# Optimization experiments

Hardware: AMD Instinct MI355X
Metric: run time of the kernel (lower is better)

The kernel has to match this reference:

```python
import jax, jax.numpy as jnp
import numpy as np


def _gnn_layer(feat, W, b, src, dst, n_nodes):
    # edge-wise: gather src feats -> Linear -> scatter-sum at dst
    m = feat @ W + b                                   # [N, out]
    agg = jax.ops.segment_sum(m[src], dst, num_segments=n_nodes)  # [N, out]
    # concat aggregated messages with self-transformed features -> 2*out
    return jnp.concatenate([agg, m], axis=-1)


def setup_inputs() -> dict:
    key = jax.random.key(0)
    ks = jax.random.split(key, 6)
    N, E, D_IN, D_OUT = 50000, 800000, 128, 128
    features = jax.random.normal(ks[0], (N, D_IN), dtype=jnp.float32)
    src = jax.random.randint(ks[1], (E,), 0, N, dtype=jnp.int32)
    dst = jax.random.randint(ks[2], (E,), 0, N, dtype=jnp.int32)
    W1 = jax.random.normal(ks[3], (D_IN, D_OUT), dtype=jnp.float32) / np.sqrt(D_IN)
    b1 = jnp.zeros((D_OUT,), dtype=jnp.float32)
    W2 = jax.random.normal(ks[4], (2 * D_OUT, D_OUT), dtype=jnp.float32) / np.sqrt(2 * D_OUT)
    b2 = jnp.zeros((D_OUT,), dtype=jnp.float32)
    return {"features": features, "src": src, "dst": dst,
            "W1": W1, "b1": b1, "W2": W2, "b2": b2}


def reference(features, src, dst, W1, b1, W2, b2):
    n_nodes = features.shape[0]
    feat = _gnn_layer(features, W1, b1, src, dst, n_nodes)  # [N, 2*out]
    feat = _gnn_layer(feat, W2, b2, src, dst, n_nodes)      # [N, 2*out]
    return feat
```

## Files before the change

### kernel.cpp

```cpp
#include <hip/hip_runtime.h>


#define D 128
#define CBLK 256
#define DCAP 8192

typedef __attribute__((ext_vector_type(8))) short short8;
typedef __attribute__((ext_vector_type(4))) float float4v;
typedef unsigned short ushort_t;
typedef unsigned int uint_t;

static __device__ __forceinline__ ushort_t f2bf(float f) {
    uint_t u = __builtin_bit_cast(uint_t, f);
    u += 0x7FFFu + ((u >> 16) & 1u);
    return (ushort_t)(u >> 16);
}
static __device__ __forceinline__ float bfhi(uint_t u) {
    return __builtin_bit_cast(float, u & 0xFFFF0000u);
}
static __device__ __forceinline__ float bflo(uint_t u) {
    return __builtin_bit_cast(float, u << 16);
}

__global__ __launch_bounds__(256) void pack_w(const float* __restrict__ W1,
                                              const float* __restrict__ W2,
                                              ushort_t* __restrict__ W1p,
                                              ushort_t* __restrict__ W2p) {
    const int n1 = 4 * 8 * 64;
    const int n2 = 8 * 8 * 64;
    int t = blockIdx.x * 256 + threadIdx.x;
    if (t >= n1 + n2) return;
    const float* W; ushort_t* Wp; int tt;
    if (t < n1) { W = W1; Wp = W1p; tt = t; }
    else        { W = W2; Wp = W2p; tt = t - n1; }
    int lane = tt & 63, cg = (tt >> 6) & 7, kb = tt >> 9;
    int krow = kb * 32 + (lane >> 4) * 8;
    int col  = cg * 16 + (lane & 15);
    #pragma unroll
    for (int j = 0; j < 8; ++j)
        Wp[(size_t)tt * 8 + j] = f2bf(W[(size_t)(krow + j) * D + col]);
}

__global__ __launch_bounds__(256) void binA(const int* __restrict__ dst,
                                            int* __restrict__ mat, int E, int NB) {
    __shared__ int h[256];
    const int c = blockIdx.x;
    for (int i = threadIdx.x; i < NB; i += 256) h[i] = 0;
    __syncthreads();
    const int chunk = (E + CBLK - 1) / CBLK;
    int e0 = c * chunk, e1 = e0 + chunk; if (e1 > E) e1 = E;
    for (int e = e0 + threadIdx.x; e < e1; e += 256)
        atomicAdd(&h[dst[e] >> 8], 1);
    __syncthreads();
    for (int i = threadIdx.x; i < NB; i += 256)
        mat[i * CBLK + c] = h[i];
}

__global__ __launch_bounds__(256) void binB1(const int* __restrict__ mat,
                                             int* __restrict__ bb,
                                             int* __restrict__ offs,
                                             int E, int N, int NB) {
    __shared__ int s[256];
    int tid = threadIdx.x;
    int v = 0;
    if (tid < NB) {
        const int* row = &mat[tid * CBLK];
        for (int c = 0; c < CBLK; ++c) v += row[c];
    }
    s[tid] = v; __syncthreads();
    for (int o = 1; o < 256; o <<= 1) {
        int t = (tid >= o) ? s[tid - o] : 0;
        __syncthreads();
        s[tid] += t;
        __syncthreads();
    }
    if (tid < NB) bb[tid] = s[tid] - v;
    if (tid == 0) { bb[NB] = E; offs[N] = E; }
}

__global__ __launch_bounds__(256) void binB2(int* __restrict__ mat,
                                             const int* __restrict__ bb, int NB) {
    __shared__ int s[256];
    int b = blockIdx.x;
    int tid = threadIdx.x;
    int v = mat[b * CBLK + tid];
    s[tid] = v; __syncthreads();
    for (int o = 1; o < 256; o <<= 1) {
        int t = (tid >= o) ? s[tid - o] : 0;
        __syncthreads();
        s[tid] += t;
        __syncthreads();
    }
    mat[b * CBLK + tid] = bb[b] + s[tid] - v;
}

__global__ __launch_bounds__(256) void binC(const int* __restrict__ src,
                                            const int* __restrict__ dst,
                                            const int* __restrict__ mat,
                                            int2* __restrict__ tmp, int E, int NB) {
    __shared__ int base[256];
    __shared__ int lcnt[256];
    const int c = blockIdx.x;
    for (int i = threadIdx.x; i < NB; i += 256) {
        base[i] = mat[i * CBLK + c];
        lcnt[i] = 0;
    }
    __syncthreads();
    const int chunk = (E + CBLK - 1) / CBLK;
    int e0 = c * chunk, e1 = e0 + chunk; if (e1 > E) e1 = E;
    for (int e = e0 + threadIdx.x; e < e1; e += 256) {
        int d = dst[e];
        int b = d >> 8;
        int p = base[b] + atomicAdd(&lcnt[b], 1);
        int2 pr; pr.x = d; pr.y = src[e];
        tmp[p] = pr;
    }
}

__global__ __launch_bounds__(256) void binD(const int2* __restrict__ tmp,
                                            const int* __restrict__ bb,
                                            int* __restrict__ offs,
                                            int* __restrict__ bsrc, int N, int NB) {
    __shared__ int hist[256];
    __shared__ int foff[256];
    __shared__ int cntf[256];
    __shared__ int outS[DCAP];
    const int b = blockIdx.x;
    const int tid = threadIdx.x;
    const int beg = bb[b], end = bb[b + 1];
    const int cnt = end - beg;
    const int n0 = b << 8;

    hist[tid] = 0;
    __syncthreads();
    for (int i = tid; i < cnt; i += 256)
        atomicAdd(&hist[tmp[beg + i].x & 255], 1);
    __syncthreads();
    int v = hist[tid];
    int s = v;
    __syncthreads();
    hist[tid] = s; __syncthreads();
    for (int o = 1; o < 256; o <<= 1) {
        int t = (tid >= o) ? hist[tid - o] : 0;
        __syncthreads();
        hist[tid] += t;
        __syncthreads();
    }
    foff[tid] = hist[tid] - v;
    cntf[tid] = 0;
    __syncthreads();

    int node = n0 + tid;
    if (node < N) offs[node] = beg + foff[tid];

    if (cnt <= DCAP) {
        for (int i = tid; i < cnt; i += 256) {
            int2 p = tmp[beg + i];
            int f = p.x & 255;
            int pos = foff[f] + atomicAdd(&cntf[f], 1);
            outS[pos] = p.y;
        }
        __syncthreads();
        for (int i = tid; i < cnt; i += 256)
            bsrc[beg + i] = outS[i];
    } else {
        for (int i = tid; i < cnt; i += 256) {
            int2 p = tmp[beg + i];
            int f = p.x & 255;
            int pos = foff[f] + atomicAdd(&cntf[f], 1);
            bsrc[beg + pos] = p.y;
        }
    }
}

__global__ __launch_bounds__(256) void gemm1_mfma(
    const float* __restrict__ X, const ushort_t* __restrict__ Wp,
    const float* __restrict__ bias, ushort_t* __restrict__ Ybf, int N)
{
    const int wave = threadIdx.x >> 6;
    const int lane = threadIdx.x & 63;
    const int quad = lane >> 4;
    const int l16  = lane & 15;
    const int r0   = blockIdx.x * 128 + wave * 32;

    float4v acc[2][8];
    #pragma unroll
    for (int cg = 0; cg < 8; ++cg) {
        float bv = bias[cg * 16 + l16];
        float4v b4 = {bv, bv, bv, bv};
        acc[0][cg] = b4; acc[1][cg] = b4;
    }

    const short8* wp8 = (const short8*)Wp;

    #pragma unroll
    for (int kb = 0; kb < 4; ++kb) {
        const int k0 = kb * 32 + quad * 8;
        short8 a[2];
        #pragma unroll
        for (int rb = 0; rb < 2; ++rb) {
            int row = r0 + rb * 16 + l16;
            if (row >= N) row = N - 1;
            const float* p = &X[(size_t)row * D + k0];
            float4 x0 = *(const float4*)p;
            float4 x1 = *(const float4*)(p + 4);
            short8 s;
            s[0] = (short)f2bf(x0.x); s[1] = (short)f2bf(x0.y);
            s[2] = (short)f2bf(x0.z); s[3] = (short)f2bf(x0.w);
            s[4] = (short)f2bf(x1.x); s[5] = (short)f2bf(x1.y);
            s[6] = (short)f2bf(x1.z); s[7] = (short)f2bf(x1.w);
            a[rb] = s;
        }
        #pragma unroll
        for (int cg = 0; cg < 8; ++cg) {
            short8 b = wp8[(kb * 8 + cg) * 64 + lane];
            acc[0][cg] = __builtin_amdgcn_mfma_f32_16x16x32_bf16(a[0], b, acc[0][cg], 0, 0, 0);
            acc[1][cg] = __builtin_amdgcn_mfma_f32_16x16x32_bf16(a[1], b, acc[1][cg], 0, 0, 0);
        }
    }

    #pragma unroll
    for (int rb = 0; rb < 2; ++rb) {
        int rowb = r0 + rb * 16 + quad * 4;
        #pragma unroll
        for (int cg = 0; cg < 8; ++cg) {
            int col = cg * 16 + l16;
            #pragma unroll
            for (int i = 0; i < 4; ++i) {
                int row = rowb + i;
                if (row < N) Ybf[(size_t)row * D + col] = f2bf(acc[rb][cg][i]);
            }
        }
    }
}

__global__ __launch_bounds__(256) void gemm2_mfma(
    const ushort_t* __restrict__ A0, const ushort_t* __restrict__ A1,
    const ushort_t* __restrict__ Wp, const float* __restrict__ bias,
    float* __restrict__ Yf, ushort_t* __restrict__ Ybf, int N)
{
    const int wave = threadIdx.x >> 6;
    const int lane = threadIdx.x & 63;
    const int quad = lane >> 4;
    const int l16  = lane & 15;
    const int r0   = blockIdx.x * 128 + wave * 32;

    float4v acc[2][8];
    #pragma unroll
    for (int cg = 0; cg < 8; ++cg) {
        float bv = bias[cg * 16 + l16];
        float4v b4 = {bv, bv, bv, bv};
        acc[0][cg] = b4; acc[1][cg] = b4;
    }

    const short8* wp8 = (const short8*)Wp;

    #pragma unroll
    for (int kb = 0; kb < 8; ++kb) {
        const ushort_t* __restrict__ A = (kb < 4) ? A0 : A1;
        const int k0 = (kb & 3) * 32 + quad * 8;
        short8 a[2];
        #pragma unroll
        for (int rb = 0; rb < 2; ++rb) {
            int row = r0 + rb * 16 + l16;
            if (row >= N) row = N - 1;
            a[rb] = *(const short8*)&A[(size_t)row * D + k0];
        }
        #pragma unroll
        for (int cg = 0; cg < 8; ++cg) {
            short8 b = wp8[(kb * 8 + cg) * 64 + lane];
            acc[0][cg] = __builtin_amdgcn_mfma_f32_16x16x32_bf16(a[0], b, acc[0][cg], 0, 0, 0);
            acc[1][cg] = __builtin_amdgcn_mfma_f32_16x16x32_bf16(a[1], b, acc[1][cg], 0, 0, 0);
        }
    }

    #pragma unroll
    for (int rb = 0; rb < 2; ++rb) {
        int rowb = r0 + rb * 16 + quad * 4;
        #pragma unroll
        for (int cg = 0; cg < 8; ++cg) {
            int col = cg * 16 + l16;
            #pragma unroll
            for (int i = 0; i < 4; ++i) {
                int row = rowb + i;
                if (row < N) {
                    float v = acc[rb][cg][i];
                    Yf[(size_t)row * 256 + col] = v;
                    Ybf[(size_t)row * D + col] = f2bf(v);
                }
            }
        }
    }
}

__global__ __launch_bounds__(256) void gather_bf(
    const ushort_t* __restrict__ msg,
    const int* __restrict__ offs, const int* __restrict__ bsrc,
    ushort_t* __restrict__ aggB,
    float* __restrict__ aggF,
    int N)
{
    int node = (blockIdx.x * 256 + threadIdx.x) >> 6;
    int lane = threadIdx.x & 63;
    if (node >= N) return;
    const int quad = lane >> 4;
    const int c16  = lane & 15;
    int beg = offs[node], end = offs[node + 1];

    float ax[4] = {0.f, 0.f, 0.f, 0.f};
    float ay[4] = {0.f, 0.f, 0.f, 0.f};
    const uint4* mp = (const uint4*)msg;

    for (int base = beg; base < end; base += 64) {
        int cnt = end - base; if (cnt > 64) cnt = 64;
        int sidx = bsrc[base + (lane < cnt ? lane : cnt - 1)];
        for (int j0 = 0; j0 < cnt; j0 += 16) {
            #pragma unroll
            for (int t = 0; t < 4; ++t) {
                int e  = j0 + t * 4 + quad;
                int ec = (e < cnt) ? e : cnt - 1;
                int s  = __shfl(sidx, ec, 64);
                uint4 u = mp[(size_t)s * 16 + c16];
                if (e < cnt) {
                    ax[0] += bflo(u.x); ay[0] += bfhi(u.x);
                    ax[1] += bflo(u.y); ay[1] += bfhi(u.y);
                    ax[2] += bflo(u.z); ay[2] += bfhi(u.z);
                    ax[3] += bflo(u.w); ay[3] += bfhi(u.w);
                }
            }
        }
    }

    #pragma unroll
    for (int k = 0; k < 4; ++k) {
        ax[k] += __shfl_xor(ax[k], 16, 64);
        ax[k] += __shfl_xor(ax[k], 32, 64);
        ay[k] += __shfl_xor(ay[k], 16, 64);
        ay[k] += __shfl_xor(ay[k], 32, 64);
    }

    if (quad == 0) {
        if (aggB) {
            uint4 o;
            o.x = (uint_t)f2bf(ax[0]) | ((uint_t)f2bf(ay[0]) << 16);
            o.y = (uint_t)f2bf(ax[1]) | ((uint_t)f2bf(ay[1]) << 16);
            o.z = (uint_t)f2bf(ax[2]) | ((uint_t)f2bf(ay[2]) << 16);
            o.w = (uint_t)f2bf(ax[3]) | ((uint_t)f2bf(ay[3]) << 16);
            ((uint4*)aggB)[(size_t)node * 16 + c16] = o;
        } else {
            float4 w0 = {ax[0], ay[0], ax[1], ay[1]};
            float4 w1 = {ax[2], ay[2], ax[3], ay[3]};
            float* p = &aggF[(size_t)node * 256 + c16 * 8];
            *(float4*)p = w0;
            *(float4*)(p + 4) = w1;
        }
    }
}

extern "C" void kernel_launch(void* const* d_in, const int* in_sizes, int n_in,
                              void* d_out, int out_size, void* d_ws, size_t ws_size,
                              hipStream_t stream) {
    const float* features = (const float*)d_in[0];
    const int*   src      = (const int*)d_in[1];
    const int*   dst      = (const int*)d_in[2];
    const float* W1       = (const float*)d_in[3];
    const float* b1       = (const float*)d_in[4];
    const float* W2       = (const float*)d_in[5];
    const float* b2       = (const float*)d_in[6];
    float* out = (float*)d_out;

    const int N = in_sizes[0] / D;
    const int E = in_sizes[1];
    const int NB = (N + 255) >> 8;

    ushort_t* m1bf   = (ushort_t*)d_ws;
    ushort_t* agg1bf = m1bf + (size_t)N * D;
    ushort_t* m2bf   = agg1bf + (size_t)N * D;
    ushort_t* W1p    = m2bf + (size_t)N * D;
    ushort_t* W2p    = W1p + 16384;
    int*  mat  = (int*)(W2p + 32768);
    int*  bb   = mat + (size_t)NB * CBLK;
    int*  offs = bb + NB + 1;
    int2* tmp  = (int2*)(offs + N + 1);
    int*  bsrc = (int*)(tmp + (size_t)E);

    const int gemmBlocks = (N + 127) / 128;

    pack_w<<<(12 * 8 * 64 + 255) / 256, 256, 0, stream>>>(W1, W2, W1p, W2p);

    binA <<<CBLK, 256, 0, stream>>>(dst, mat, E, NB);
    binB1<<<1,    256, 0, stream>>>(mat, bb, offs, E, N, NB);
    binB2<<<NB,   256, 0, stream>>>(mat, bb, NB);
    binC <<<CBLK, 256, 0, stream>>>(src, dst, mat, tmp, E, NB);
    binD <<<NB,   256, 0, stream>>>(tmp, bb, offs, bsrc, N, NB);

    gemm1_mfma<<<gemmBlocks, 256, 0, stream>>>(features, W1p, b1, m1bf, N);
    gather_bf<<<(N * 64 + 255) / 256, 256, 0, stream>>>(m1bf, offs, bsrc,
                                                        agg1bf, nullptr, N);
    gemm2_mfma<<<gemmBlocks, 256, 0, stream>>>(agg1bf, m1bf, W2p, b2,
                                               out + D, m2bf, N);
    gather_bf<<<(N * 64 + 255) / 256, 256, 0, stream>>>(m2bf, offs, bsrc,
                                                        nullptr, out, N);
}
```

Baseline: 213.3 us.

## Merge preprocessing kernels and fuse layer-1 aggregation into the second GEMM

Merges weight packing with the dst histogram and the edge scatter with the first GEMM as block-partitioned kernels, and folds the two prefix-scan kernels into one kernel where each block recomputes the global bucket scan. The first-layer gather now runs inside the second GEMM: each block aggregates its 128 nodes into swizzled shared memory and feeds that tile straight to MFMA. This drops several launches and the agg1 round trip through global memory. In exchange the GEMM2 blocks take on irregular gather work and use more LDS, which may lower occupancy.

```diff
diff --git a/kernel.cpp b/kernel.cpp
--- a/kernel.cpp
+++ b/kernel.cpp
@@ -22,13 +22,28 @@
     return __builtin_bit_cast(float, u << 16);
 }
 
-__global__ __launch_bounds__(256) void pack_w(const float* __restrict__ W1,
-                                              const float* __restrict__ W2,
-                                              ushort_t* __restrict__ W1p,
-                                              ushort_t* __restrict__ W2p) {
+__global__ __launch_bounds__(256) void packw_binA(
+    const float* __restrict__ W1, const float* __restrict__ W2,
+    ushort_t* __restrict__ W1p, ushort_t* __restrict__ W2p,
+    const int* __restrict__ dst, int* __restrict__ mat, int E, int NB)
+{
+    __shared__ int h[256];
+    if (blockIdx.x < CBLK) {
+        const int c = blockIdx.x;
+        for (int i = threadIdx.x; i < NB; i += 256) h[i] = 0;
+        __syncthreads();
+        const int chunk = (E + CBLK - 1) / CBLK;
+        int e0 = c * chunk, e1 = e0 + chunk; if (e1 > E) e1 = E;
+        for (int e = e0 + threadIdx.x; e < e1; e += 256)
+            atomicAdd(&h[dst[e] >> 8], 1);
+        __syncthreads();
+        for (int i = threadIdx.x; i < NB; i += 256)
+            mat[i * CBLK + c] = h[i];
+        return;
+    }
     const int n1 = 4 * 8 * 64;
     const int n2 = 8 * 8 * 64;
-    int t = blockIdx.x * 256 + threadIdx.x;
+    int t = (blockIdx.x - CBLK) * 256 + threadIdx.x;
     if (t >= n1 + n2) return;
     const float* W; ushort_t* Wp; int tt;
     if (t < n1) { W = W1; Wp = W1p; tt = t; }
@@ -41,27 +56,15 @@
         Wp[(size_t)tt * 8 + j] = f2bf(W[(size_t)(krow + j) * D + col]);
 }
 
-__global__ __launch_bounds__(256) void binA(const int* __restrict__ dst,
-                                            int* __restrict__ mat, int E, int NB) {
-    __shared__ int h[256];
-    const int c = blockIdx.x;
-    for (int i = threadIdx.x; i < NB; i += 256) h[i] = 0;
-    __syncthreads();
-    const int chunk = (E + CBLK - 1) / CBLK;
-    int e0 = c * chunk, e1 = e0 + chunk; if (e1 > E) e1 = E;
-    for (int e = e0 + threadIdx.x; e < e1; e += 256)
-        atomicAdd(&h[dst[e] >> 8], 1);
-    __syncthreads();
-    for (int i = threadIdx.x; i < NB; i += 256)
-        mat[i * CBLK + c] = h[i];
-}
-
-__global__ __launch_bounds__(256) void binB1(const int* __restrict__ mat,
-                                             int* __restrict__ bb,
-                                             int* __restrict__ offs,
-                                             int E, int N, int NB) {
+__global__ __launch_bounds__(256) void binB(
+    const int* __restrict__ mat, int* __restrict__ matc,
+    int* __restrict__ bb, int* __restrict__ offs, int E, int N, int NB)
+{
     __shared__ int s[256];
-    int tid = threadIdx.x;
+    __shared__ int ex[256];
+    const int b = blockIdx.x;
+    const int tid = threadIdx.x;
+
     int v = 0;
     if (tid < NB) {
         const int* row = &mat[tid * CBLK];
@@ -74,46 +77,107 @@
         s[tid] += t;
         __syncthreads();
     }
-    if (tid < NB) bb[tid] = s[tid] - v;
-    if (tid == 0) { bb[NB] = E; offs[N] = E; }
-}
-
-__global__ __launch_bounds__(256) void binB2(int* __restrict__ mat,
-                                             const int* __restrict__ bb, int NB) {
-    __shared__ int s[256];
-    int b = blockIdx.x;
-    int tid = threadIdx.x;
-    int v = mat[b * CBLK + tid];
-    s[tid] = v; __syncthreads();
+    ex[tid] = s[tid] - v;
+    __syncthreads();
+    if (b == 0) {
+        if (tid < NB) bb[tid] = ex[tid];
+        if (tid == 0) { bb[NB] = E; offs[N] = E; }
+    }
+    const int bbb = ex[b];
+
+    int v2 = mat[b * CBLK + tid];
+    __syncthreads();
+    s[tid] = v2; __syncthreads();
     for (int o = 1; o < 256; o <<= 1) {
         int t = (tid >= o) ? s[tid - o] : 0;
         __syncthreads();
         s[tid] += t;
         __syncthreads();
     }
-    mat[b * CBLK + tid] = bb[b] + s[tid] - v;
-}
-
-__global__ __launch_bounds__(256) void binC(const int* __restrict__ src,
-                                            const int* __restrict__ dst,
-                                            const int* __restrict__ mat,
-                                            int2* __restrict__ tmp, int E, int NB) {
+    matc[b * CBLK + tid] = bbb + s[tid] - v2;
+}
+
+__global__ __launch_bounds__(256) void binC_gemm1(
+    const int* __restrict__ src, const int* __restrict__ dst,
+    const int* __restrict__ matc, int2* __restrict__ tmp, int E, int NB,
+    const float* __restrict__ X, const ushort_t* __restrict__ Wp,
+    const float* __restrict__ bias, ushort_t* __restrict__ Ybf, int N)
+{
     __shared__ int base[256];
     __shared__ int lcnt[256];
-    const int c = blockIdx.x;
-    for (int i = threadIdx.x; i < NB; i += 256) {
-        base[i] = mat[i * CBLK + c];
-        lcnt[i] = 0;
-    }
-    __syncthreads();
-    const int chunk = (E + CBLK - 1) / CBLK;
-    int e0 = c * chunk, e1 = e0 + chunk; if (e1 > E) e1 = E;
-    for (int e = e0 + threadIdx.x; e < e1; e += 256) {
-        int d = dst[e];
-        int b = d >> 8;
-        int p = base[b] + atomicAdd(&lcnt[b], 1);
-        int2 pr; pr.x = d; pr.y = src[e];
-        tmp[p] = pr;
+    if (blockIdx.x < CBLK) {
+        const int c = blockIdx.x;
+        for (int i = threadIdx.x; i < NB; i += 256) {
+            base[i] = matc[i * CBLK + c];
+            lcnt[i] = 0;
+        }
+        __syncthreads();
+        const int chunk = (E + CBLK - 1) / CBLK;
+        int e0 = c * chunk, e1 = e0 + chunk; if (e1 > E) e1 = E;
+        for (int e = e0 + threadIdx.x; e < e1; e += 256) {
+            int d = dst[e];
+            int b = d >> 8;
+            int p = base[b] + atomicAdd(&lcnt[b], 1);
+            int2 pr; pr.x = d; pr.y = src[e];
+            tmp[p] = pr;
+        }
+        return;
+    }
+
+    const int wave = threadIdx.x >> 6;
+    const int lane = threadIdx.x & 63;
+    const int quad = lane >> 4;
+    const int l16  = lane & 15;
+    const int r0   = (blockIdx.x - CBLK) * 128 + wave * 32;
+
+    float4v acc[2][8];
+    #pragma unroll
+    for (int cg = 0; cg < 8; ++cg) {
+        float bv = bias[cg * 16 + l16];
+        float4v b4 = {bv, bv, bv, bv};
+        acc[0][cg] = b4; acc[1][cg] = b4;
+    }
+
+    const short8* wp8 = (const short8*)Wp;
+
+    #pragma unroll
+    for (int kb = 0; kb < 4; ++kb) {
+        const int k0 = kb * 32 + quad * 8;
+        short8 a[2];
+        #pragma unroll
+        for (int rb = 0; rb < 2; ++rb) {
+            int row = r0 + rb * 16 + l16;
+            if (row >= N) row = N - 1;
+            const float* p = &X[(size_t)row * D + k0];
+            float4 x0 = *(const float4*)p;
+            float4 x1 = *(const float4*)(p + 4);
+            short8 s;
+            s[0] = (short)f2bf(x0.x); s[1] = (short)f2bf(x0.y);
+            s[2] = (short)f2bf(x0.z); s[3] = (short)f2bf(x0.w);
+            s[4] = (short)f2bf(x1.x); s[5] = (short)f2bf(x1.y);
+            s[6] = (short)f2bf(x1.z); s[7] = (short)f2bf(x1.w);
+            a[rb] = s;
+        }
+        #pragma unroll
+        for (int cg = 0; cg < 8; ++cg) {
+            short8 b = wp8[(kb * 8 + cg) * 64 + lane];
+            acc[0][cg] = __builtin_amdgcn_mfma_f32_16x16x32_bf16(a[0], b, acc[0][cg], 0, 0, 0);
+            acc[1][cg] = __builtin_amdgcn_mfma_f32_16x16x32_bf16(a[1], b, acc[1][cg], 0, 0, 0);
+        }
+    }
+
+    #pragma unroll
+    for (int rb = 0; rb < 2; ++rb) {
+        int rowb = r0 + rb * 16 + quad * 4;
+        #pragma unroll
+        for (int cg = 0; cg < 8; ++cg) {
+            int col = cg * 16 + l16;
+            #pragma unroll
+            for (int i = 0; i < 4; ++i) {
+                int row = rowb + i;
+                if (row < N) Ybf[(size_t)row * D + col] = f2bf(acc[rb][cg][i]);
+            }
+        }
     }
 }
 
@@ -137,9 +201,8 @@
         atomicAdd(&hist[tmp[beg + i].x & 255], 1);
     __syncthreads();
     int v = hist[tid];
-    int s = v;
-    __syncthreads();
-    hist[tid] = s; __syncthreads();
+    __syncthreads();
+    hist[tid] = v; __syncthreads();
     for (int o = 1; o < 256; o <<= 1) {
         int t = (tid >= o) ? hist[tid - o] : 0;
         __syncthreads();
@@ -173,15 +236,75 @@
     }
 }
 
-__global__ __launch_bounds__(256) void gemm1_mfma(
-    const float* __restrict__ X, const ushort_t* __restrict__ Wp,
-    const float* __restrict__ bias, ushort_t* __restrict__ Ybf, int N)
+__global__ __launch_bounds__(256) void gemm2_fused(
+    const ushort_t* __restrict__ m1bf,
+    const int* __restrict__ offs, const int* __restrict__ bsrc,
+    const ushort_t* __restrict__ Wp, const float* __restrict__ bias,
+    float* __restrict__ Yf, ushort_t* __restrict__ Ybf, int N)
 {
-    const int wave = threadIdx.x >> 6;
-    const int lane = threadIdx.x & 63;
+    __shared__ uint4 aggS4[128 * 16];
+    __shared__ int offsS[129];
+
+    const int tid  = threadIdx.x;
+    const int wave = tid >> 6;
+    const int lane = tid & 63;
     const int quad = lane >> 4;
     const int l16  = lane & 15;
-    const int r0   = blockIdx.x * 128 + wave * 32;
+    const int c16  = l16;
+    const int n0   = blockIdx.x * 128;
+    int nv = N - n0; if (nv > 128) nv = 128;
+
+    for (int t = tid; t <= nv; t += 256) offsS[t] = offs[n0 + t];
+    {
+        uint4 z; z.x = z.y = z.z = z.w = 0u;
+        for (int r = nv + (tid >> 4); r < 128; r += 16)
+            aggS4[r * 16 + (tid & 15)] = z;
+    }
+    __syncthreads();
+
+    const uint4* mp = (const uint4*)m1bf;
+    for (int i = wave; i < nv; i += 4) {
+        int beg = offsS[i], end = offsS[i + 1];
+        float ax[4] = {0.f, 0.f, 0.f, 0.f};
+        float ay[4] = {0.f, 0.f, 0.f, 0.f};
+        for (int base = beg; base < end; base += 64) {
+            int cnt = end - base; if (cnt > 64) cnt = 64;
+            int sidx = bsrc[base + (lane < cnt ? lane : cnt - 1)];
+            for (int j0 = 0; j0 < cnt; j0 += 16) {
+                #pragma unroll
+                for (int t = 0; t < 4; ++t) {
+                    int e  = j0 + t * 4 + quad;
+                    int ec = (e < cnt) ? e : cnt - 1;
+                    int s  = __shfl(sidx, ec, 64);
+                    uint4 u = mp[(size_t)s * 16 + c16];
+                    if (e < cnt) {
+                        ax[0] += bflo(u.x); ay[0] += bfhi(u.x);
+                        ax[1] += bflo(u.y); ay[1] += bfhi(u.y);
+                        ax[2] += bflo(u.z); ay[2] += bfhi(u.z);
+                        ax[3] += bflo(u.w); ay[3] += bfhi(u.w);
+                    }
+                }
+            }
+        }
+        #pragma unroll
+        for (int k = 0; k < 4; ++k) {
+            ax[k] += __shfl_xor(ax[k], 16, 64);
+            ax[k] += __shfl_xor(ax[k], 32, 64);
+            ay[k] += __shfl_xor(ay[k], 16, 64);
+            ay[k] += __shfl_xor(ay[k], 32, 64);
+        }
+        if (quad == 0) {
+            uint4 o;
+            o.x = (uint_t)f2bf(ax[0]) | ((uint_t)f2bf(ay[0]) << 16);
+            o.y = (uint_t)f2bf(ax[1]) | ((uint_t)f2bf(ay[1]) << 16);
+            o.z = (uint_t)f2bf(ax[2]) | ((uint_t)f2bf(ay[2]) << 16);
+            o.w = (uint_t)f2bf(ax[3]) | ((uint_t)f2bf(ay[3]) << 16);
+            aggS4[i * 16 + (c16 ^ (i & 15))] = o;
+        }
+    }
+    __syncthreads();
+
+    const int r0 = n0 + wave * 32;
 
     float4v acc[2][8];
     #pragma unroll
@@ -192,79 +315,26 @@
     }
 
     const short8* wp8 = (const short8*)Wp;
-
-    #pragma unroll
-    for (int kb = 0; kb < 4; ++kb) {
-        const int k0 = kb * 32 + quad * 8;
-        short8 a[2];
-        #pragma unroll
-        for (int rb = 0; rb < 2; ++rb) {
-            int row = r0 + rb * 16 + l16;
-            if (row >= N) row = N - 1;
-            const float* p = &X[(size_t)row * D + k0];
-            float4 x0 = *(const float4*)p;
-            float4 x1 = *(const float4*)(p + 4);
-            short8 s;
-            s[0] = (short)f2bf(x0.x); s[1] = (short)f2bf(x0.y);
-            s[2] = (short)f2bf(x0.z); s[3] = (short)f2bf(x0.w);
-            s[4] = (short)f2bf(x1.x); s[5] = (short)f2bf(x1.y);
-            s[6] = (short)f2bf(x1.z); s[7] = (short)f2bf(x1.w);
-            a[rb] = s;
-        }
-        #pragma unroll
-        for (int cg = 0; cg < 8; ++cg) {
-            short8 b = wp8[(kb * 8 + cg) * 64 + lane];
-            acc[0][cg] = __builtin_amdgcn_mfma_f32_16x16x32_bf16(a[0], b, acc[0][cg], 0, 0, 0);
-            acc[1][cg] = __builtin_amdgcn_mfma_f32_16x16x32_bf16(a[1], b, acc[1][cg], 0, 0, 0);
-        }
-    }
-
-    #pragma unroll
-    for (int rb = 0; rb < 2; ++rb) {
-        int rowb = r0 + rb * 16 + quad * 4;
-        #pragma unroll
-        for (int cg = 0; cg < 8; ++cg) {
-            int col = cg * 16 + l16;
-            #pragma unroll
-            for (int i = 0; i < 4; ++i) {
-                int row = rowb + i;
-                if (row < N) Ybf[(size_t)row * D + col] = f2bf(acc[rb][cg][i]);
-            }
-        }
-    }
-}
-
-__global__ __launch_bounds__(256) void gemm2_mfma(
-    const ushort_t* __restrict__ A0, const ushort_t* __restrict__ A1,
-    const ushort_t* __restrict__ Wp, const float* __restrict__ bias,
-    float* __restrict__ Yf, ushort_t* __restrict__ Ybf, int N)
-{
-    const int wave = threadIdx.x >> 6;
-    const int lane = threadIdx.x & 63;
-    const int quad = lane >> 4;
-    const int l16  = lane & 15;
-    const int r0   = blockIdx.x * 128 + wave * 32;
-
-    float4v acc[2][8];
-    #pragma unroll
-    for (int cg = 0; cg < 8; ++cg) {
-        float bv = bias[cg * 16 + l16];
-        float4v b4 = {bv, bv, bv, bv};
-        acc[0][cg] = b4; acc[1][cg] = b4;
-    }
-
-    const short8* wp8 = (const short8*)Wp;
+    const short8* aggS8 = (const short8*)aggS4;
 
     #pragma unroll
     for (int kb = 0; kb < 8; ++kb) {
-        const ushort_t* __restrict__ A = (kb < 4) ? A0 : A1;
         const int k0 = (kb & 3) * 32 + quad * 8;
         short8 a[2];
-        #pragma unroll
-        for (int rb = 0; rb < 2; ++rb) {
-            int row = r0 + rb * 16 + l16;
-            if (row >= N) row = N - 1;
-            a[rb] = *(const short8*)&A[(size_t)row * D + k0];
+        if (kb < 4) {
+            const int g = (kb & 3) * 4 + quad;
+            #pragma unroll
+            for (int rb = 0; rb < 2; ++rb) {
+                int li = wave * 32 + rb * 16 + l16;
+                a[rb] = aggS8[li * 16 + (g ^ (li & 15))];
+            }
+        } else {
+            #pragma unroll
+            for (int rb = 0; rb < 2; ++rb) {
+                int row = r0 + rb * 16 + l16;
+                if (row >= N) row = N - 1;
+                a[rb] = *(const short8*)&m1bf[(size_t)row * D + k0];
+            }
         }
         #pragma unroll
         for (int cg = 0; cg < 8; ++cg) {
@@ -296,7 +366,6 @@
 __global__ __launch_bounds__(256) void gather_bf(
     const ushort_t* __restrict__ msg,
     const int* __restrict__ offs, const int* __restrict__ bsrc,
-    ushort_t* __restrict__ aggB,
     float* __restrict__ aggF,
     int N)
 {
@@ -340,20 +409,11 @@
     }
 
     if (quad == 0) {
-        if (aggB) {
-            uint4 o;
-            o.x = (uint_t)f2bf(ax[0]) | ((uint_t)f2bf(ay[0]) << 16);
-            o.y = (uint_t)f2bf(ax[1]) | ((uint_t)f2bf(ay[1]) << 16);
-            o.z = (uint_t)f2bf(ax[2]) | ((uint_t)f2bf(ay[2]) << 16);
-            o.w = (uint_t)f2bf(ax[3]) | ((uint_t)f2bf(ay[3]) << 16);
-            ((uint4*)aggB)[(size_t)node * 16 + c16] = o;
-        } else {
-            float4 w0 = {ax[0], ay[0], ax[1], ay[1]};
-            float4 w1 = {ax[2], ay[2], ax[3], ay[3]};
-            float* p = &aggF[(size_t)node * 256 + c16 * 8];
-            *(float4*)p = w0;
-            *(float4*)(p + 4) = w1;
-        }
+        float4 w0 = {ax[0], ay[0], ax[1], ay[1]};
+        float4 w1 = {ax[2], ay[2], ax[3], ay[3]};
+        float* p = &aggF[(size_t)node * 256 + c16 * 8];
+        *(float4*)p = w0;
+        *(float4*)(p + 4) = w1;
     }
 }
 
@@ -373,32 +433,25 @@
     const int E = in_sizes[1];
     const int NB = (N + 255) >> 8;
 
-    ushort_t* m1bf   = (ushort_t*)d_ws;
-    ushort_t* agg1bf = m1bf + (size_t)N * D;
-    ushort_t* m2bf   = agg1bf + (size_t)N * D;
-    ushort_t* W1p    = m2bf + (size_t)N * D;
-    ushort_t* W2p    = W1p + 16384;
+    ushort_t* m1bf = (ushort_t*)d_ws;
+    ushort_t* m2bf = m1bf + (size_t)N * D;
+    ushort_t* W1p  = m2bf + (size_t)N * D;
+    ushort_t* W2p  = W1p + 16384;
     int*  mat  = (int*)(W2p + 32768);
-    int*  bb   = mat + (size_t)NB * CBLK;
+    int*  matc = mat + (size_t)NB * CBLK;
+    int*  bb   = matc + (size_t)NB * CBLK;
     int*  offs = bb + NB + 1;
     int2* tmp  = (int2*)(offs + N + 1);
     int*  bsrc = (int*)(tmp + (size_t)E);
 
     const int gemmBlocks = (N + 127) / 128;
 
-    pack_w<<<(12 * 8 * 64 + 255) / 256, 256, 0, stream>>>(W1, W2, W1p, W2p);
-
-    binA <<<CBLK, 256, 0, stream>>>(dst, mat, E, NB);
-    binB1<<<1,    256, 0, stream>>>(mat, bb, offs, E, N, NB);
-    binB2<<<NB,   256, 0, stream>>>(mat, bb, NB);
-    binC <<<CBLK, 256, 0, stream>>>(src, dst, mat, tmp, E, NB);
-    binD <<<NB,   256, 0, stream>>>(tmp, bb, offs, bsrc, N, NB);
-
-    gemm1_mfma<<<gemmBlocks, 256, 0, stream>>>(features, W1p, b1, m1bf, N);
-    gather_bf<<<(N * 64 + 255) / 256, 256, 0, stream>>>(m1bf, offs, bsrc,
-                                                        agg1bf, nullptr, N);
-    gemm2_mfma<<<gemmBlocks, 256, 0, stream>>>(agg1bf, m1bf, W2p, b2,
-                                               out + D, m2bf, N);
-    gather_bf<<<(N * 64 + 255) / 256, 256, 0, stream>>>(m2bf, offs, bsrc,
-                                                        nullptr, out, N);
-}
+    packw_binA<<<CBLK + 24, 256, 0, stream>>>(W1, W2, W1p, W2p, dst, mat, E, NB);
+    binB<<<NB, 256, 0, stream>>>(mat, matc, bb, offs, E, N, NB);
+    binC_gemm1<<<CBLK + gemmBlocks, 256, 0, stream>>>(src, dst, matc, tmp, E, NB,
+                                                      features, W1p, b1, m1bf, N);
+    binD<<<NB, 256, 0, stream>>>(tmp, bb, offs, bsrc, N, NB);
+    gemm2_fused<<<gemmBlocks, 256, 0, stream>>>(m1bf, offs, bsrc, W2p, b2,
+                                                out + D, m2bf, N);
+    gather_bf<<<(N * 64 + 255) / 256, 256, 0, stream>>>(m2bf, offs, bsrc, out, N);
+}
```

Result: slower. 254.0 us (+19.0%).

## Merge preprocessing launches: fuse pack_w with binA, binB1/B2, binC with gemm1

Applied to the files above, without the earlier changes.

Cuts the launch count from 9 to 6 by running independent work in a single grid. Weight packing shares a grid with the dst histogram, and the first GEMM shares a grid with the edge scatter, with block-index ranges choosing the role. The two scan kernels become one, where every block redoes the bucket-total scan and writes its column prefix into a separate matc buffer so no in-place race can occur. This removes launch gaps and inter-kernel serialization, at the cost of redundant scan work and extra workspace.

```diff
diff --git a/kernel.cpp b/kernel.cpp
--- a/kernel.cpp
+++ b/kernel.cpp
@@ -22,13 +22,28 @@
     return __builtin_bit_cast(float, u << 16);
 }
 
-__global__ __launch_bounds__(256) void pack_w(const float* __restrict__ W1,
-                                              const float* __restrict__ W2,
-                                              ushort_t* __restrict__ W1p,
-                                              ushort_t* __restrict__ W2p) {
+__global__ __launch_bounds__(256) void packw_binA(
+    const float* __restrict__ W1, const float* __restrict__ W2,
+    ushort_t* __restrict__ W1p, ushort_t* __restrict__ W2p,
+    const int* __restrict__ dst, int* __restrict__ mat, int E, int NB)
+{
+    __shared__ int h[256];
+    if (blockIdx.x < CBLK) {
+        const int c = blockIdx.x;
+        for (int i = threadIdx.x; i < NB; i += 256) h[i] = 0;
+        __syncthreads();
+        const int chunk = (E + CBLK - 1) / CBLK;
+        int e0 = c * chunk, e1 = e0 + chunk; if (e1 > E) e1 = E;
+        for (int e = e0 + threadIdx.x; e < e1; e += 256)
+            atomicAdd(&h[dst[e] >> 8], 1);
+        __syncthreads();
+        for (int i = threadIdx.x; i < NB; i += 256)
+            mat[i * CBLK + c] = h[i];
+        return;
+    }
     const int n1 = 4 * 8 * 64;
     const int n2 = 8 * 8 * 64;
-    int t = blockIdx.x * 256 + threadIdx.x;
+    int t = (blockIdx.x - CBLK) * 256 + threadIdx.x;
     if (t >= n1 + n2) return;
     const float* W; ushort_t* Wp; int tt;
     if (t < n1) { W = W1; Wp = W1p; tt = t; }
@@ -41,27 +56,15 @@
         Wp[(size_t)tt * 8 + j] = f2bf(W[(size_t)(krow + j) * D + col]);
 }
 
-__global__ __launch_bounds__(256) void binA(const int* __restrict__ dst,
-                                            int* __restrict__ mat, int E, int NB) {
-    __shared__ int h[256];
-    const int c = blockIdx.x;
-    for (int i = threadIdx.x; i < NB; i += 256) h[i] = 0;
-    __syncthreads();
-    const int chunk = (E + CBLK - 1) / CBLK;
-    int e0 = c * chunk, e1 = e0 + chunk; if (e1 > E) e1 = E;
-    for (int e = e0 + threadIdx.x; e < e1; e += 256)
-        atomicAdd(&h[dst[e] >> 8], 1);
-    __syncthreads();
-    for (int i = threadIdx.x; i < NB; i += 256)
-        mat[i * CBLK + c] = h[i];
-}
-
-__global__ __launch_bounds__(256) void binB1(const int* __restrict__ mat,
-                                             int* __restrict__ bb,
-                                             int* __restrict__ offs,
-                                             int E, int N, int NB) {
+__global__ __launch_bounds__(256) void binB(
+    const int* __restrict__ mat, int* __restrict__ matc,
+    int* __restrict__ bb, int* __restrict__ offs, int E, int N, int NB)
+{
     __shared__ int s[256];
-    int tid = threadIdx.x;
+    __shared__ int ex[256];
+    const int b = blockIdx.x;
+    const int tid = threadIdx.x;
+
     int v = 0;
     if (tid < NB) {
         const int* row = &mat[tid * CBLK];
@@ -74,46 +77,107 @@
         s[tid] += t;
         __syncthreads();
     }
-    if (tid < NB) bb[tid] = s[tid] - v;
-    if (tid == 0) { bb[NB] = E; offs[N] = E; }
-}
-
-__global__ __launch_bounds__(256) void binB2(int* __restrict__ mat,
-                                             const int* __restrict__ bb, int NB) {
-    __shared__ int s[256];
-    int b = blockIdx.x;
-    int tid = threadIdx.x;
-    int v = mat[b * CBLK + tid];
-    s[tid] = v; __syncthreads();
+    ex[tid] = s[tid] - v;
+    __syncthreads();
+    if (b == 0) {
+        if (tid < NB) bb[tid] = ex[tid];
+        if (tid == 0) { bb[NB] = E; offs[N] = E; }
+    }
+    const int bbb = ex[b];
+
+    int v2 = mat[b * CBLK + tid];
+    __syncthreads();
+    s[tid] = v2; __syncthreads();
     for (int o = 1; o < 256; o <<= 1) {
         int t = (tid >= o) ? s[tid - o] : 0;
         __syncthreads();
         s[tid] += t;
         __syncthreads();
     }
-    mat[b * CBLK + tid] = bb[b] + s[tid] - v;
-}
-
-__global__ __launch_bounds__(256) void binC(const int* __restrict__ src,
-                                            const int* __restrict__ dst,
-                                            const int* __restrict__ mat,
-                                            int2* __restrict__ tmp, int E, int NB) {
+    matc[b * CBLK + tid] = bbb + s[tid] - v2;
+}
+
+__global__ __launch_bounds__(256) void binC_gemm1(
+    const int* __restrict__ src, const int* __restrict__ dst,
+    const int* __restrict__ matc, int2* __restrict__ tmp, int E, int NB,
+    const float* __restrict__ X, const ushort_t* __restrict__ Wp,
+    const float* __restrict__ bias, ushort_t* __restrict__ Ybf, int N)
+{
     __shared__ int base[256];
     __shared__ int lcnt[256];
-    const int c = blockIdx.x;
-    for (int i = threadIdx.x; i < NB; i += 256) {
-        base[i] = mat[i * CBLK + c];
-        lcnt[i] = 0;
-    }
-    __syncthreads();
-    const int chunk = (E + CBLK - 1) / CBLK;
-    int e0 = c * chunk, e1 = e0 + chunk; if (e1 > E) e1 = E;
-    for (int e = e0 + threadIdx.x; e < e1; e += 256) {
-        int d = dst[e];
-        int b = d >> 8;
-        int p = base[b] + atomicAdd(&lcnt[b], 1);
-        int2 pr; pr.x = d; pr.y = src[e];
-        tmp[p] = pr;
+    if (blockIdx.x < CBLK) {
+        const int c = blockIdx.x;
+        for (int i = threadIdx.x; i < NB; i += 256) {
+            base[i] = matc[i * CBLK + c];
+            lcnt[i] = 0;
+        }
+        __syncthreads();
+        const int chunk = (E + CBLK - 1) / CBLK;
+        int e0 = c * chunk, e1 = e0 + chunk; if (e1 > E) e1 = E;
+        for (int e = e0 + threadIdx.x; e < e1; e += 256) {
+            int d = dst[e];
+            int b = d >> 8;
+            int p = base[b] + atomicAdd(&lcnt[b], 1);
+            int2 pr; pr.x = d; pr.y = src[e];
+            tmp[p] = pr;
+        }
+        return;
+    }
+
+    const int wave = threadIdx.x >> 6;
+    const int lane = threadIdx.x & 63;
+    const int quad = lane >> 4;
+    const int l16  = lane & 15;
+    const int r0   = (blockIdx.x - CBLK) * 128 + wave * 32;
+
+    float4v acc[2][8];
+    #pragma unroll
+    for (int cg = 0; cg < 8; ++cg) {
+        float bv = bias[cg * 16 + l16];
+        float4v b4 = {bv, bv, bv, bv};
+        acc[0][cg] = b4; acc[1][cg] = b4;
+    }
+
+    const short8* wp8 = (const short8*)Wp;
+
+    #pragma unroll
+    for (int kb = 0; kb < 4; ++kb) {
+        const int k0 = kb * 32 + quad * 8;
+        short8 a[2];
+        #pragma unroll
+        for (int rb = 0; rb < 2; ++rb) {
+            int row = r0 + rb * 16 + l16;
+            if (row >= N) row = N - 1;
+            const float* p = &X[(size_t)row * D + k0];
+            float4 x0 = *(const float4*)p;
+            float4 x1 = *(const float4*)(p + 4);
+            short8 s;
+            s[0] = (short)f2bf(x0.x); s[1] = (short)f2bf(x0.y);
+            s[2] = (short)f2bf(x0.z); s[3] = (short)f2bf(x0.w);
+            s[4] = (short)f2bf(x1.x); s[5] = (short)f2bf(x1.y);
+            s[6] = (short)f2bf(x1.z); s[7] = (short)f2bf(x1.w);
+            a[rb] = s;
+        }
+        #pragma unroll
+        for (int cg = 0; cg < 8; ++cg) {
+            short8 b = wp8[(kb * 8 + cg) * 64 + lane];
+            acc[0][cg] = __builtin_amdgcn_mfma_f32_16x16x32_bf16(a[0], b, acc[0][cg], 0, 0, 0);
+            acc[1][cg] = __builtin_amdgcn_mfma_f32_16x16x32_bf16(a[1], b, acc[1][cg], 0, 0, 0);
+        }
+    }
+
+    #pragma unroll
+    for (int rb = 0; rb < 2; ++rb) {
+        int rowb = r0 + rb * 16 + quad * 4;
+        #pragma unroll
+        for (int cg = 0; cg < 8; ++cg) {
+            int col = cg * 16 + l16;
+            #pragma unroll
+            for (int i = 0; i < 4; ++i) {
+                int row = rowb + i;
+                if (row < N) Ybf[(size_t)row * D + col] = f2bf(acc[rb][cg][i]);
+            }
+        }
     }
 }
 
@@ -137,9 +201,8 @@
         atomicAdd(&hist[tmp[beg + i].x & 255], 1);
     __syncthreads();
     int v = hist[tid];
-    int s = v;
-    __syncthreads();
-    hist[tid] = s; __syncthreads();
+    __syncthreads();
+    hist[tid] = v; __syncthreads();
     for (int o = 1; o < 256; o <<= 1) {
         int t = (tid >= o) ? hist[tid - o] : 0;
         __syncthreads();
@@ -169,67 +232,6 @@
             int f = p.x & 255;
             int pos = foff[f] + atomicAdd(&cntf[f], 1);
             bsrc[beg + pos] = p.y;
-        }
-    }
-}
-
-__global__ __launch_bounds__(256) void gemm1_mfma(
-    const float* __restrict__ X, const ushort_t* __restrict__ Wp,
-    const float* __restrict__ bias, ushort_t* __restrict__ Ybf, int N)
-{
-    const int wave = threadIdx.x >> 6;
-    const int lane = threadIdx.x & 63;
-    const int quad = lane >> 4;
-    const int l16  = lane & 15;
-    const int r0   = blockIdx.x * 128 + wave * 32;
-
-    float4v acc[2][8];
-    #pragma unroll
-    for (int cg = 0; cg < 8; ++cg) {
-        float bv = bias[cg * 16 + l16];
-        float4v b4 = {bv, bv, bv, bv};
-        acc[0][cg] = b4; acc[1][cg] = b4;
-    }
-
-    const short8* wp8 = (const short8*)Wp;
-
-    #pragma unroll
-    for (int kb = 0; kb < 4; ++kb) {
-        const int k0 = kb * 32 + quad * 8;
-        short8 a[2];
-        #pragma unroll
-        for (int rb = 0; rb < 2; ++rb) {
-            int row = r0 + rb * 16 + l16;
-            if (row >= N) row = N - 1;
-            const float* p = &X[(size_t)row * D + k0];
-            float4 x0 = *(const float4*)p;
-            float4 x1 = *(const float4*)(p + 4);
-            short8 s;
-            s[0] = (short)f2bf(x0.x); s[1] = (short)f2bf(x0.y);
-            s[2] = (short)f2bf(x0.z); s[3] = (short)f2bf(x0.w);
-            s[4] = (short)f2bf(x1.x); s[5] = (short)f2bf(x1.y);
-            s[6] = (short)f2bf(x1.z); s[7] = (short)f2bf(x1.w);
-            a[rb] = s;
-        }
-        #pragma unroll
-        for (int cg = 0; cg < 8; ++cg) {
-            short8 b = wp8[(kb * 8 + cg) * 64 + lane];
-            acc[0][cg] = __builtin_amdgcn_mfma_f32_16x16x32_bf16(a[0], b, acc[0][cg], 0, 0, 0);
-            acc[1][cg] = __builtin_amdgcn_mfma_f32_16x16x32_bf16(a[1], b, acc[1][cg], 0, 0, 0);
-        }
-    }
-
-    #pragma unroll
-    for (int rb = 0; rb < 2; ++rb) {
-        int rowb = r0 + rb * 16 + quad * 4;
-        #pragma unroll
-        for (int cg = 0; cg < 8; ++cg) {
-            int col = cg * 16 + l16;
-            #pragma unroll
-            for (int i = 0; i < 4; ++i) {
-                int row = rowb + i;
-                if (row < N) Ybf[(size_t)row * D + col] = f2bf(acc[rb][cg][i]);
-            }
         }
     }
 }
@@ -379,22 +381,19 @@
     ushort_t* W1p    = m2bf + (size_t)N * D;
     ushort_t* W2p    = W1p + 16384;
     int*  mat  = (int*)(W2p + 32768);
-    int*  bb   = mat + (size_t)NB * CBLK;
+    int*  matc = mat + (size_t)NB * CBLK;
+    int*  bb   = matc + (size_t)NB * CBLK;
     int*  offs = bb + NB + 1;
     int2* tmp  = (int2*)(offs + N + 1);
     int*  bsrc = (int*)(tmp + (size_t)E);
 
     const int gemmBlocks = (N + 127) / 128;
 
-    pack_w<<<(12 * 8 * 64 + 255) / 256, 256, 0, stream>>>(W1, W2, W1p, W2p);
-
-    binA <<<CBLK, 256, 0, stream>>>(dst, mat, E, NB);
-    binB1<<<1,    256, 0, stream>>>(mat, bb, offs, E, N, NB);
-    binB2<<<NB,   256, 0, stream>>>(mat, bb, NB);
-    binC <<<CBLK, 256, 0, stream>>>(src, dst, mat, tmp, E, NB);
-    binD <<<NB,   256, 0, stream>>>(tmp, bb, offs, bsrc, N, NB);
-
-    gemm1_mfma<<<gemmBlocks, 256, 0, stream>>>(features, W1p, b1, m1bf, N);
+    packw_binA<<<CBLK + 24, 256, 0, stream>>>(W1, W2, W1p, W2p, dst, mat, E, NB);
+    binB<<<NB, 256, 0, stream>>>(mat, matc, bb, offs, E, N, NB);
+    binC_gemm1<<<CBLK + gemmBlocks, 256, 0, stream>>>(src, dst, matc, tmp, E, NB,
+                                                      features, W1p, b1, m1bf, N);
+    binD<<<NB, 256, 0, stream>>>(tmp, bb, offs, bsrc, N, NB);
     gather_bf<<<(N * 64 + 255) / 256, 256, 0, stream>>>(m1bf, offs, bsrc,
                                                         agg1bf, nullptr, N);
     gemm2_mfma<<<gemmBlocks, 256, 0, stream>>>(agg1bf, m1bf, W2p, b2,
```

Result: faster. 208.5 us (-2.3%).
